# Kernel tuning notes

Measured on AMD Instinct MI355X. Metric: run time of the kernel, lower is better.

The kernel has to match this reference:

```python
import jax, jax.numpy as jnp
import numpy as np

DIM = 33
BATCH, W, H = 8, 1024, 1024


def _identity_lut(dim):
    # Matches IdentityLUT33.txt: flat index n = i*dim^2 + j*dim + k holds
    # (r, g, b) = (k, j, i)/(dim-1), i.e. r varies fastest.
    g = jnp.arange(dim, dtype=jnp.float32) / (dim - 1)
    lut = jnp.stack([
        jnp.broadcast_to(g[None, None, :], (dim, dim, dim)),  # R channel
        jnp.broadcast_to(g[None, :, None], (dim, dim, dim)),  # G channel
        jnp.broadcast_to(g[:, None, None], (dim, dim, dim)),  # B channel
    ])
    return lut  # [3, dim, dim, dim]


def setup_inputs() -> dict:
    key = jax.random.key(0)
    LUT = _identity_lut(DIM)
    x = jax.random.uniform(key, (BATCH, 3, W, H), dtype=jnp.float32)
    return {"LUT": LUT, "x": x}


def reference(LUT, x):
    # x: [B, 3, W, H] with values in [0, 1]; LUT: [3, dim, dim, dim]
    dim = LUT.shape[-1]
    binsize = 1.0001 / (dim - 1)  # guarantees floor index <= dim-2 for x <= 1
    scaled = x / binsize
    idx = jnp.floor(scaled).astype(jnp.int32)   # bin indices per channel
    frac = scaled - idx                          # trilinear fractions
    r0, g0, b0 = idx[:, 0], idx[:, 1], idx[:, 2]   # each [B, W, H]
    rd, gd, bd = frac[:, 0], frac[:, 1], frac[:, 2]

    def corner(dr, dg, db):
        # CUDA kernel: flat id = r + g*dim + b*dim^2 within each channel,
        # so [3,d,d,d] LUT is indexed LUT[c, b, g, r]. Result: [3, B, W, H].
        return LUT[:, b0 + db, g0 + dg, r0 + dr]

    out = (((1 - rd) * (1 - gd) * (1 - bd))[None] * corner(0, 0, 0)
           + (rd * (1 - gd) * (1 - bd))[None] * corner(1, 0, 0)
           + ((1 - rd) * gd * (1 - bd))[None] * corner(0, 1, 0)
           + (rd * gd * (1 - bd))[None] * corner(1, 1, 0)
           + ((1 - rd) * (1 - gd) * bd)[None] * corner(0, 0, 1)
           + (rd * (1 - gd) * bd)[None] * corner(1, 0, 1)
           + ((1 - rd) * gd * bd)[None] * corner(0, 1, 1)
           + (rd * gd * bd)[None] * corner(1, 1, 1))
    return jnp.transpose(out, (1, 0, 2, 3))  # [B, 3, W, H]
```

## Files before the change

kernel.cpp:

```cpp
#include <hip/hip_runtime.h>


namespace {

constexpr int DIM    = 33;
constexpr int WH     = 1024 * 1024;
constexpr int BATCH  = 8;
constexpr int NPIX   = BATCH * WH;
constexpr int LUT_N  = DIM * DIM * DIM;
constexpr size_t WS_PACKED = (size_t)LUT_N * sizeof(unsigned int);

__global__ __launch_bounds__(256) void pack_kernel(
    const float* __restrict__ lut, unsigned int* __restrict__ ws)
{
    int i = blockIdx.x * blockDim.x + threadIdx.x;
    if (i >= LUT_N) return;
    float r = lut[i];
    float g = lut[LUT_N + i];
    float b = lut[2 * LUT_N + i];
    unsigned int qr = (unsigned int)__float2int_rn(__saturatef(r) * 1023.0f);
    unsigned int qg = (unsigned int)__float2int_rn(__saturatef(g) * 1023.0f);
    unsigned int qb = (unsigned int)__float2int_rn(__saturatef(b) * 1023.0f);
    ws[i] = qr | (qg << 10) | (qb << 20);
}

__device__ __forceinline__ void sample_one_lds(
    const unsigned int* __restrict__ lds_lut, float r, float g, float b,
    float& outR, float& outG, float& outB)
{
    const float inv_binsize = 32.0f / 1.0001f;
    float sr = r * inv_binsize;
    float sg = g * inv_binsize;
    float sb = b * inv_binsize;
    int ir = (int)sr, ig = (int)sg, ib = (int)sb;
    float fr = sr - (float)ir;
    float fg = sg - (float)ig;
    float fb = sb - (float)ib;

    int base = ib * (DIM * DIM) + ig * DIM + ir;

    unsigned int p000 = lds_lut[base];
    unsigned int p100 = lds_lut[base + 1];
    unsigned int p010 = lds_lut[base + DIM];
    unsigned int p110 = lds_lut[base + DIM + 1];
    unsigned int p001 = lds_lut[base + DIM * DIM];
    unsigned int p101 = lds_lut[base + DIM * DIM + 1];
    unsigned int p011 = lds_lut[base + DIM * DIM + DIM];
    unsigned int p111 = lds_lut[base + DIM * DIM + DIM + 1];

    float w00 = (1.f - fg) * (1.f - fb);
    float w10 = fg * (1.f - fb);
    float w01 = (1.f - fg) * fb;
    float w11 = fg * fb;
    float w000 = (1.f - fr) * w00, w100 = fr * w00;
    float w010 = (1.f - fr) * w10, w110 = fr * w10;
    float w001 = (1.f - fr) * w01, w101 = fr * w01;
    float w011 = (1.f - fr) * w11, w111 = fr * w11;

    float accR, accG, accB;
    accR  = w000 * (float)(p000 & 1023u);
    accG  = w000 * (float)((p000 >> 10) & 1023u);
    accB  = w000 * (float)((p000 >> 20) & 1023u);
    accR += w100 * (float)(p100 & 1023u);
    accG += w100 * (float)((p100 >> 10) & 1023u);
    accB += w100 * (float)((p100 >> 20) & 1023u);
    accR += w010 * (float)(p010 & 1023u);
    accG += w010 * (float)((p010 >> 10) & 1023u);
    accB += w010 * (float)((p010 >> 20) & 1023u);
    accR += w110 * (float)(p110 & 1023u);
    accG += w110 * (float)((p110 >> 10) & 1023u);
    accB += w110 * (float)((p110 >> 20) & 1023u);
    accR += w001 * (float)(p001 & 1023u);
    accG += w001 * (float)((p001 >> 10) & 1023u);
    accB += w001 * (float)((p001 >> 20) & 1023u);
    accR += w101 * (float)(p101 & 1023u);
    accG += w101 * (float)((p101 >> 10) & 1023u);
    accB += w101 * (float)((p101 >> 20) & 1023u);
    accR += w011 * (float)(p011 & 1023u);
    accG += w011 * (float)((p011 >> 10) & 1023u);
    accB += w011 * (float)((p011 >> 20) & 1023u);
    accR += w111 * (float)(p111 & 1023u);
    accG += w111 * (float)((p111 >> 10) & 1023u);
    accB += w111 * (float)((p111 >> 20) & 1023u);

    const float inv1023 = 1.0f / 1023.0f;
    outR = accR * inv1023;
    outG = accG * inv1023;
    outB = accB * inv1023;
}

__global__ __launch_bounds__(1024, 1) void lut3d_lds_kernel(
    const unsigned int* __restrict__ packed, const float* __restrict__ x,
    float* __restrict__ out)
{
    __shared__ unsigned int lds_lut[LUT_N];

    for (int i = threadIdx.x; i < LUT_N; i += 1024)
        lds_lut[i] = packed[i];
    __syncthreads();

    const int nthreads = gridDim.x * 1024;
    const int ngroups  = NPIX / 4;

    for (int gid = blockIdx.x * 1024 + threadIdx.x; gid < ngroups; gid += nthreads) {
        int P = gid * 4;
        int batch = P >> 20;
        int p = P & (WH - 1);

        const float* xb = x + (size_t)batch * 3 * WH + p;
        float*       ob = out + (size_t)batch * 3 * WH + p;

        float4 r4 = *(const float4*)(xb);
        float4 g4 = *(const float4*)(xb + WH);
        float4 b4 = *(const float4*)(xb + 2 * WH);

        float4 oR, oG, oB;
        sample_one_lds(lds_lut, r4.x, g4.x, b4.x, oR.x, oG.x, oB.x);
        sample_one_lds(lds_lut, r4.y, g4.y, b4.y, oR.y, oG.y, oB.y);
        sample_one_lds(lds_lut, r4.z, g4.z, b4.z, oR.z, oG.z, oB.z);
        sample_one_lds(lds_lut, r4.w, g4.w, b4.w, oR.w, oG.w, oB.w);

        *(float4*)(ob)          = oR;
        *(float4*)(ob + WH)     = oG;
        *(float4*)(ob + 2 * WH) = oB;
    }
}

__global__ __launch_bounds__(256) void repack_kernel(
    const float* __restrict__ lut, float4* __restrict__ ws)
{
    int i = blockIdx.x * blockDim.x + threadIdx.x;
    if (i >= LUT_N) return;
    float4 v;
    v.x = lut[i];
    v.y = lut[LUT_N + i];
    v.z = lut[2 * LUT_N + i];
    v.w = 0.f;
    ws[i] = v;
}

__device__ __forceinline__ void sample_one_g(
    const float4* __restrict__ lut4, float r, float g, float b,
    float& outR, float& outG, float& outB)
{
    const float inv_binsize = 32.0f / 1.0001f;
    float sr = r * inv_binsize, sg = g * inv_binsize, sb = b * inv_binsize;
    int ir = (int)sr, ig = (int)sg, ib = (int)sb;
    float fr = sr - (float)ir, fg = sg - (float)ig, fb = sb - (float)ib;
    int base = ib * (DIM * DIM) + ig * DIM + ir;
    const float4 c000 = lut4[base];
    const float4 c100 = lut4[base + 1];
    const float4 c010 = lut4[base + DIM];
    const float4 c110 = lut4[base + DIM + 1];
    const float4 c001 = lut4[base + DIM * DIM];
    const float4 c101 = lut4[base + DIM * DIM + 1];
    const float4 c011 = lut4[base + DIM * DIM + DIM];
    const float4 c111 = lut4[base + DIM * DIM + DIM + 1];
    float w00 = (1.f - fg) * (1.f - fb);
    float w10 = fg * (1.f - fb);
    float w01 = (1.f - fg) * fb;
    float w11 = fg * fb;
    float w000 = (1.f - fr) * w00, w100 = fr * w00;
    float w010 = (1.f - fr) * w10, w110 = fr * w10;
    float w001 = (1.f - fr) * w01, w101 = fr * w01;
    float w011 = (1.f - fr) * w11, w111 = fr * w11;
    outR = w000 * c000.x + w100 * c100.x + w010 * c010.x + w110 * c110.x
         + w001 * c001.x + w101 * c101.x + w011 * c011.x + w111 * c111.x;
    outG = w000 * c000.y + w100 * c100.y + w010 * c010.y + w110 * c110.y
         + w001 * c001.y + w101 * c101.y + w011 * c011.y + w111 * c111.y;
    outB = w000 * c000.z + w100 * c100.z + w010 * c010.z + w110 * c110.z
         + w001 * c001.z + w101 * c101.z + w011 * c011.z + w111 * c111.z;
}

__global__ __launch_bounds__(256) void lut3d_kernel_g(
    const float4* __restrict__ lut4, const float* __restrict__ x,
    float* __restrict__ out)
{
    int tid = blockIdx.x * blockDim.x + threadIdx.x;
    int P = tid * 4;
    if (P >= NPIX) return;
    int batch = P >> 20;
    int p = P & (WH - 1);
    const float* xb = x + (size_t)batch * 3 * WH + p;
    float*       ob = out + (size_t)batch * 3 * WH + p;
    float4 r4 = *(const float4*)(xb);
    float4 g4 = *(const float4*)(xb + WH);
    float4 b4 = *(const float4*)(xb + 2 * WH);
    float4 oR, oG, oB;
    sample_one_g(lut4, r4.x, g4.x, b4.x, oR.x, oG.x, oB.x);
    sample_one_g(lut4, r4.y, g4.y, b4.y, oR.y, oG.y, oB.y);
    sample_one_g(lut4, r4.z, g4.z, b4.z, oR.z, oG.z, oB.z);
    sample_one_g(lut4, r4.w, g4.w, b4.w, oR.w, oG.w, oB.w);
    *(float4*)(ob)          = oR;
    *(float4*)(ob + WH)     = oG;
    *(float4*)(ob + 2 * WH) = oB;
}

}

extern "C" void kernel_launch(void* const* d_in, const int* in_sizes, int n_in,
                              void* d_out, int out_size, void* d_ws, size_t ws_size,
                              hipStream_t stream) {
    const float* lut = (const float*)d_in[0];
    const float* x   = (const float*)d_in[1];
    float*       out = (float*)d_out;

    if (ws_size >= WS_PACKED) {
        unsigned int* packed = (unsigned int*)d_ws;
        pack_kernel<<<(LUT_N + 255) / 256, 256, 0, stream>>>(lut, packed);
        lut3d_lds_kernel<<<256, 1024, 0, stream>>>(packed, x, out);
    } else if (ws_size >= (size_t)LUT_N * sizeof(float4)) {
        float4* lut4 = (float4*)d_ws;
        repack_kernel<<<(LUT_N + 255) / 256, 256, 0, stream>>>(lut, lut4);
        constexpr int grid = (NPIX / 4 + 255) / 256;
        lut3d_kernel_g<<<grid, 256, 0, stream>>>(lut4, x, out);
    }
}
```

Measured before the change: 223.0 us.

## Fuse LUT packing into main kernel, software-prefetch inputs, use nontemporal memory ops

Removes the separate pack kernel launch; each block now quantizes the LUT from global memory directly into LDS. The grid-stride loop becomes a fully unrolled fixed-count loop that loads the next iteration's pixel inputs before computing the current one, so global loads overlap with LDS gathers and math. Input loads and output stores use nontemporal builtins to avoid polluting the cache with streaming data. In exchange, every block repeats the packing work (strided three-channel reads), register pressure rises from holding two sets of inputs, and the workspace fallback path is removed.

```diff
diff --git a/kernel.cpp b/kernel.cpp
--- a/kernel.cpp
+++ b/kernel.cpp
@@ -8,24 +8,24 @@
 constexpr int BATCH  = 8;
 constexpr int NPIX   = BATCH * WH;
 constexpr int LUT_N  = DIM * DIM * DIM;
-constexpr size_t WS_PACKED = (size_t)LUT_N * sizeof(unsigned int);
 
-__global__ __launch_bounds__(256) void pack_kernel(
-    const float* __restrict__ lut, unsigned int* __restrict__ ws)
-{
-    int i = blockIdx.x * blockDim.x + threadIdx.x;
-    if (i >= LUT_N) return;
-    float r = lut[i];
-    float g = lut[LUT_N + i];
-    float b = lut[2 * LUT_N + i];
-    unsigned int qr = (unsigned int)__float2int_rn(__saturatef(r) * 1023.0f);
-    unsigned int qg = (unsigned int)__float2int_rn(__saturatef(g) * 1023.0f);
-    unsigned int qb = (unsigned int)__float2int_rn(__saturatef(b) * 1023.0f);
-    ws[i] = qr | (qg << 10) | (qb << 20);
+constexpr int BLOCKS  = 256;
+constexpr int TPB     = 1024;
+constexpr int NTHREAD = BLOCKS * TPB;
+constexpr int NGROUP  = NPIX / 4;
+constexpr int NITER   = NGROUP / NTHREAD;
+
+using f4 = __attribute__((ext_vector_type(4))) float;
+
+__device__ __forceinline__ f4 nt_load4(const float* p) {
+    return __builtin_nontemporal_load((const f4*)p);
+}
+__device__ __forceinline__ void nt_store4(float* p, f4 v) {
+    __builtin_nontemporal_store(v, (f4*)p);
 }
 
 __device__ __forceinline__ void sample_one_lds(
-    const unsigned int* __restrict__ lds_lut, float r, float g, float b,
+    const unsigned int* lds_lut, float r, float g, float b,
     float& outR, float& outG, float& outB)
 {
     const float inv_binsize = 32.0f / 1.0001f;
@@ -89,111 +89,67 @@
     outB = accB * inv1023;
 }
 
-__global__ __launch_bounds__(1024, 1) void lut3d_lds_kernel(
-    const unsigned int* __restrict__ packed, const float* __restrict__ x,
+__global__ __launch_bounds__(TPB, 1) void lut3d_lds_kernel(
+    const float* __restrict__ lut, const float* __restrict__ x,
     float* __restrict__ out)
 {
     __shared__ unsigned int lds_lut[LUT_N];
 
-    for (int i = threadIdx.x; i < LUT_N; i += 1024)
-        lds_lut[i] = packed[i];
+    for (int i = threadIdx.x; i < LUT_N; i += TPB) {
+        float r = lut[i];
+        float g = lut[LUT_N + i];
+        float b = lut[2 * LUT_N + i];
+        unsigned int qr = (unsigned int)__float2int_rn(__saturatef(r) * 1023.0f);
+        unsigned int qg = (unsigned int)__float2int_rn(__saturatef(g) * 1023.0f);
+        unsigned int qb = (unsigned int)__float2int_rn(__saturatef(b) * 1023.0f);
+        lds_lut[i] = qr | (qg << 10) | (qb << 20);
+    }
     __syncthreads();
 
-    const int nthreads = gridDim.x * 1024;
-    const int ngroups  = NPIX / 4;
+    int gid = blockIdx.x * TPB + threadIdx.x;
 
-    for (int gid = blockIdx.x * 1024 + threadIdx.x; gid < ngroups; gid += nthreads) {
-        int P = gid * 4;
-        int batch = P >> 20;
-        int p = P & (WH - 1);
-
-        const float* xb = x + (size_t)batch * 3 * WH + p;
-        float*       ob = out + (size_t)batch * 3 * WH + p;
-
-        float4 r4 = *(const float4*)(xb);
-        float4 g4 = *(const float4*)(xb + WH);
-        float4 b4 = *(const float4*)(xb + 2 * WH);
-
-        float4 oR, oG, oB;
-        sample_one_lds(lds_lut, r4.x, g4.x, b4.x, oR.x, oG.x, oB.x);
-        sample_one_lds(lds_lut, r4.y, g4.y, b4.y, oR.y, oG.y, oB.y);
-        sample_one_lds(lds_lut, r4.z, g4.z, b4.z, oR.z, oG.z, oB.z);
-        sample_one_lds(lds_lut, r4.w, g4.w, b4.w, oR.w, oG.w, oB.w);
-
-        *(float4*)(ob)          = oR;
-        *(float4*)(ob + WH)     = oG;
-        *(float4*)(ob + 2 * WH) = oB;
-    }
-}
-
-__global__ __launch_bounds__(256) void repack_kernel(
-    const float* __restrict__ lut, float4* __restrict__ ws)
-{
-    int i = blockIdx.x * blockDim.x + threadIdx.x;
-    if (i >= LUT_N) return;
-    float4 v;
-    v.x = lut[i];
-    v.y = lut[LUT_N + i];
-    v.z = lut[2 * LUT_N + i];
-    v.w = 0.f;
-    ws[i] = v;
-}
-
-__device__ __forceinline__ void sample_one_g(
-    const float4* __restrict__ lut4, float r, float g, float b,
-    float& outR, float& outG, float& outB)
-{
-    const float inv_binsize = 32.0f / 1.0001f;
-    float sr = r * inv_binsize, sg = g * inv_binsize, sb = b * inv_binsize;
-    int ir = (int)sr, ig = (int)sg, ib = (int)sb;
-    float fr = sr - (float)ir, fg = sg - (float)ig, fb = sb - (float)ib;
-    int base = ib * (DIM * DIM) + ig * DIM + ir;
-    const float4 c000 = lut4[base];
-    const float4 c100 = lut4[base + 1];
-    const float4 c010 = lut4[base + DIM];
-    const float4 c110 = lut4[base + DIM + 1];
-    const float4 c001 = lut4[base + DIM * DIM];
-    const float4 c101 = lut4[base + DIM * DIM + 1];
-    const float4 c011 = lut4[base + DIM * DIM + DIM];
-    const float4 c111 = lut4[base + DIM * DIM + DIM + 1];
-    float w00 = (1.f - fg) * (1.f - fb);
-    float w10 = fg * (1.f - fb);
-    float w01 = (1.f - fg) * fb;
-    float w11 = fg * fb;
-    float w000 = (1.f - fr) * w00, w100 = fr * w00;
-    float w010 = (1.f - fr) * w10, w110 = fr * w10;
-    float w001 = (1.f - fr) * w01, w101 = fr * w01;
-    float w011 = (1.f - fr) * w11, w111 = fr * w11;
-    outR = w000 * c000.x + w100 * c100.x + w010 * c010.x + w110 * c110.x
-         + w001 * c001.x + w101 * c101.x + w011 * c011.x + w111 * c111.x;
-    outG = w000 * c000.y + w100 * c100.y + w010 * c010.y + w110 * c110.y
-         + w001 * c001.y + w101 * c101.y + w011 * c011.y + w111 * c111.y;
-    outB = w000 * c000.z + w100 * c100.z + w010 * c010.z + w110 * c110.z
-         + w001 * c001.z + w101 * c101.z + w011 * c011.z + w111 * c111.z;
-}
-
-__global__ __launch_bounds__(256) void lut3d_kernel_g(
-    const float4* __restrict__ lut4, const float* __restrict__ x,
-    float* __restrict__ out)
-{
-    int tid = blockIdx.x * blockDim.x + threadIdx.x;
-    int P = tid * 4;
-    if (P >= NPIX) return;
+    int P = gid * 4;
     int batch = P >> 20;
     int p = P & (WH - 1);
     const float* xb = x + (size_t)batch * 3 * WH + p;
-    float*       ob = out + (size_t)batch * 3 * WH + p;
-    float4 r4 = *(const float4*)(xb);
-    float4 g4 = *(const float4*)(xb + WH);
-    float4 b4 = *(const float4*)(xb + 2 * WH);
-    float4 oR, oG, oB;
-    sample_one_g(lut4, r4.x, g4.x, b4.x, oR.x, oG.x, oB.x);
-    sample_one_g(lut4, r4.y, g4.y, b4.y, oR.y, oG.y, oB.y);
-    sample_one_g(lut4, r4.z, g4.z, b4.z, oR.z, oG.z, oB.z);
-    sample_one_g(lut4, r4.w, g4.w, b4.w, oR.w, oG.w, oB.w);
-    *(float4*)(ob)          = oR;
-    *(float4*)(ob + WH)     = oG;
-    *(float4*)(ob + 2 * WH) = oB;
+    f4 r4 = nt_load4(xb);
+    f4 g4 = nt_load4(xb + WH);
+    f4 b4 = nt_load4(xb + 2 * WH);
+
+#pragma unroll
+    for (int it = 0; it < NITER; ++it) {
+        f4 rn, gn, bn;
+        int gnx = gid + NTHREAD;
+        if (it + 1 < NITER) {
+            int Pn = gnx * 4;
+            int bn_ = Pn >> 20;
+            int pn  = Pn & (WH - 1);
+            const float* xn = x + (size_t)bn_ * 3 * WH + pn;
+            rn = nt_load4(xn);
+            gn = nt_load4(xn + WH);
+            bn = nt_load4(xn + 2 * WH);
+        }
+
+        float* ob = out + (size_t)batch * 3 * WH + p;
+
+        f4 oR, oG, oB;
+#pragma unroll
+        for (int l = 0; l < 4; ++l) {
+            float tR, tG, tB;
+            sample_one_lds(lds_lut, r4[l], g4[l], b4[l], tR, tG, tB);
+            oR[l] = tR; oG[l] = tG; oB[l] = tB;
+        }
+
+        nt_store4(ob,          oR);
+        nt_store4(ob + WH,     oG);
+        nt_store4(ob + 2 * WH, oB);
+
+        gid = gnx;
+        P = gid * 4;
+        batch = P >> 20;
+        p = P & (WH - 1);
+        r4 = rn; g4 = gn; b4 = bn;
+    }
 }
 
 }
@@ -204,15 +160,7 @@
     const float* lut = (const float*)d_in[0];
     const float* x   = (const float*)d_in[1];
     float*       out = (float*)d_out;
+    (void)d_ws; (void)ws_size;
 
-    if (ws_size >= WS_PACKED) {
-        unsigned int* packed = (unsigned int*)d_ws;
-        pack_kernel<<<(LUT_N + 255) / 256, 256, 0, stream>>>(lut, packed);
-        lut3d_lds_kernel<<<256, 1024, 0, stream>>>(packed, x, out);
-    } else if (ws_size >= (size_t)LUT_N * sizeof(float4)) {
-        float4* lut4 = (float4*)d_ws;
-        repack_kernel<<<(LUT_N + 255) / 256, 256, 0, stream>>>(lut, lut4);
-        constexpr int grid = (NPIX / 4 + 255) / 256;
-        lut3d_kernel_g<<<grid, 256, 0, stream>>>(lut4, x, out);
-    }
+    lut3d_lds_kernel<<<BLOCKS, TPB, 0, stream>>>(lut, x, out);
 }
```

After: 186.3 us. -16.5%, faster.
